# Kernel tuning notes

Hardware: AMD Instinct MI355X
Metric: run time of the kernel (lower is better)

## Reference

```python
import jax, jax.numpy as jnp
jax.config.update("jax_enable_x64", True)
import numpy as np

VOXEL_SIZE = 0.1   # size_scheduler.value
VBITS = 12         # bits per voxel coordinate (signed, offset by VOFF)
VMASK = (1 << VBITS) - 1
VOFF = 1 << (VBITS - 1)
GBITS = 10         # bits for group index (G=1024)


def setup_inputs() -> dict:
    key = jax.random.key(0)
    B, G, P, F = 64, 1024, 64, 3
    active_pred = jax.random.normal(key, (B * G, P, F), dtype=jnp.float32)
    active_mask = jnp.ones((B, G), dtype=bool)  # all active -> static nonzero count
    return {"active_pred": active_pred, "active_mask": active_mask}


def reference(active_pred, active_mask):
    N, P, F = active_pred.shape
    # active_mask.nonzero() -> [N, 2] (batch, group) ids
    bi, gi = jnp.nonzero(active_mask, size=N)
    bg = jnp.stack([bi, gi], axis=1).astype(jnp.int64)              # [N, 2]
    bg = jnp.broadcast_to(bg[:, None, :], (N, P, 2)).reshape(-1, 2)  # [N*P, 2]
    offsets = active_pred.reshape(-1, F)[:, :3]                      # [N*P, 3]
    vox = jnp.floor(offsets / VOXEL_SIZE).astype(jnp.int64)          # [N*P, 3]
    # Pack (b, g, vx, vy, vz) into one int64 key; packing is lexicographic-order
    # preserving, so sorted-unique of codes == torch.unique(dim=0) row order.
    v = vox + VOFF                                                   # nonnegative
    code = ((((bg[:, 0] << GBITS) | bg[:, 1]) << (3 * VBITS))
            | (v[:, 0] << (2 * VBITS)) | (v[:, 1] << VBITS) | v[:, 2])
    ucode, cluster_indices = jnp.unique(
        code, return_inverse=True, size=code.shape[0], fill_value=jnp.max(code))
    # Decode unique codes back to [U, 5] keys (padded tail repeats max key).
    ub = ucode >> (3 * VBITS + GBITS)
    ug = (ucode >> (3 * VBITS)) & ((1 << GBITS) - 1)
    uv0 = ((ucode >> (2 * VBITS)) & VMASK) - VOFF
    uv1 = ((ucode >> VBITS) & VMASK) - VOFF
    uv2 = (ucode & VMASK) - VOFF
    unique_keys = jnp.stack([ub, ug, uv0, uv1, uv2], axis=1)
    return unique_keys, cluster_indices
```

## Files before the change

### kernel.cpp

```cpp
#include <hip/hip_runtime.h>
#include <cstdint>

typedef unsigned long long u64;
typedef unsigned int u32;

constexpr int VBITS = 12;
constexpr int VOFF  = 1 << (VBITS - 1);
constexpr int GBITS = 10;

constexpr int GPB = 16;
constexpr int WPB = 4;
constexpr int GPW = 4;

__device__ inline u32 wave_sort_u32(u32 k, int lane) {
    #pragma unroll
    for (int ks = 2; ks <= 64; ks <<= 1) {
        #pragma unroll
        for (int j = ks >> 1; j >= 1; j >>= 1) {
            u32 other = __shfl_xor(k, j, 64);
            bool takeMin = ((lane & ks) == 0) == ((lane & j) == 0);
            u32 mn = min(k, other), mx = max(k, other);
            k = takeMin ? mn : mx;
        }
    }
    return k;
}

__device__ inline u64 wave_sort_u64(u64 k, int lane) {
    #pragma unroll
    for (int ks = 2; ks <= 64; ks <<= 1) {
        #pragma unroll
        for (int j = ks >> 1; j >= 1; j >>= 1) {
            u64 other = __shfl_xor(k, j, 64);
            bool takeMin = ((lane & ks) == 0) == ((lane & j) == 0);
            u64 mn = k < other ? k : other;
            u64 mx = k < other ? other : k;
            k = takeMin ? mn : mx;
        }
    }
    return k;
}

__device__ inline u64 voxel_code_u64(float x, float y, float z) {
    long long v0 = (long long)floorf(x / 0.1f) + VOFF;
    long long v1 = (long long)floorf(y / 0.1f) + VOFF;
    long long v2 = (long long)floorf(z / 0.1f) + VOFF;
    return ((u64)v0 << 24) | ((u64)v1 << 12) | (u64)v2;
}

__global__ __launch_bounds__(256) void vox_build(
    const float* __restrict__ pred,
    u32* __restrict__ keys32,
    u64* __restrict__ meta,
    u32* __restrict__ counts,
    u32* __restrict__ blockSums,
    int ngroups)
{
    __shared__ float sf[GPB * 192];
    __shared__ u32 s_ws[WPB];
    const int t = threadIdx.x, w = t >> 6, lane = t & 63, b = blockIdx.x;

    {
        const float4* p4 = (const float4*)pred + (size_t)b * (GPB * 48);
        const size_t f4tot = (size_t)ngroups * 48;
        float4* s4 = (float4*)sf;
        #pragma unroll
        for (int i = 0; i < 3; i++) {
            int idx = t + i * 256;
            size_t gidx = (size_t)b * (GPB * 48) + idx;
            if (gidx < f4tot) s4[idx] = p4[idx];
        }
    }
    __syncthreads();

    u32 wsum = 0;
    for (int j = 0; j < GPW; ++j) {
        int gi = w * GPW + j, gid = b * GPB + gi;
        if (gid >= ngroups) break;

        const float* q = sf + gi * 192 + lane * 3;
        int v0 = (int)floorf(q[0] / 0.1f) + VOFF;
        int v1 = (int)floorf(q[1] / 0.1f) + VOFF;
        int v2 = (int)floorf(q[2] / 0.1f) + VOFF;

        int r0 = __shfl(v0, 0, 64), r1 = __shfl(v1, 0, 64), r2 = __shfl(v2, 0, 64);
        int d0 = v0 - r0 + 128, d1 = v1 - r1 + 128, d2 = v2 - r2 + 128;
        bool bad = ((u32)(d0 | d1 | d2) > 255u) || ((u32)(v0 | v1 | v2) > 4095u);

        u32 cnt, outk;
        if (!__any(bad)) {
            u32 k = ((u32)d0 << 22) | ((u32)d1 << 14) | ((u32)d2 << 6) | (u32)lane;
            k = wave_sort_u32(k, lane);
            u32 sk = k >> 6, pv = __shfl_up(sk, 1, 64);
            int flag = (lane == 0 || sk != pv) ? 1 : 0;
            cnt = (u32)__popcll(__ballot(flag));
            outk = k;
            if (lane == 0)
                meta[gid] = ((u64)((u32)(r0 - 128) & 4095))
                          | ((u64)((u32)(r1 - 128) & 4095) << 12)
                          | ((u64)((u32)(r2 - 128) & 4095) << 24);
        } else {
            u64 code = ((u64)(long long)v0 << 24) | ((u64)(long long)v1 << 12)
                     | (u64)(long long)v2;
            u64 k = wave_sort_u64((code << 6) | (u64)lane, lane);
            u64 sk = k >> 6, pv = __shfl_up(sk, 1, 64);
            int flag = (lane == 0 || sk != pv) ? 1 : 0;
            cnt = (u32)__popcll(__ballot(flag));
            outk = (u32)(k & 63);
            if (lane == 0) meta[gid] = (1ull << 48);
        }
        keys32[(size_t)gid * 64 + lane] = outk;
        if (lane == 0) counts[gid] = cnt;
        wsum += cnt;
    }
    if (lane == 0) s_ws[w] = wsum;
    __syncthreads();
    if (t == 0) blockSums[b] = s_ws[0] + s_ws[1] + s_ws[2] + s_ws[3];
}

__global__ __launch_bounds__(256) void vox_emit(
    const float* __restrict__ pred,
    const u32* __restrict__ keys32,
    const u64* __restrict__ meta,
    const u32* __restrict__ counts,
    const u32* __restrict__ blockSums,
    int* __restrict__ okeys,
    int* __restrict__ inv,
    int ngroups, int totalrows, int nblocks)
{
    __shared__ u32 s_k[GPB * 64];
    __shared__ u32 s_c[GPB];
    __shared__ u64 s_m[GPB];
    __shared__ int s_stage[WPB][320];
    __shared__ u32 s_baseU[2];
    __shared__ int s_tail[5];
    const int t = threadIdx.x, w = t >> 6, lane = t & 63, b = blockIdx.x;

    {
        const uint4* k4 = (const uint4*)keys32 + (size_t)b * (GPB * 16);
        const size_t k4tot = (size_t)ngroups * 16;
        size_t gidx = (size_t)b * (GPB * 16) + t;
        if (gidx < k4tot) ((uint4*)s_k)[t] = k4[t];
    }
    if (t < GPB) {
        int gid = b * GPB + t;
        s_c[t] = (gid < ngroups) ? counts[gid] : 0;
        s_m[t] = (gid < ngroups) ? meta[gid] : 0;
    }

    {
        u32 below = 0, all = 0;
        for (int i = t; i < nblocks; i += 256) {
            u32 v = blockSums[i];
            all += v;
            if (i < b) below += v;
        }
        u32* scratch = (u32*)&s_stage[0][0];
        scratch[t] = below; scratch[256 + t] = all;
        __syncthreads();
        #pragma unroll
        for (int off = 128; off >= 1; off >>= 1) {
            if (t < off) {
                scratch[t]       += scratch[t + off];
                scratch[256 + t] += scratch[256 + t + off];
            }
            __syncthreads();
        }
        if (t == 0) { s_baseU[0] = scratch[0]; s_baseU[1] = scratch[256]; }
        __syncthreads();
    }

    u32 base = s_baseU[0];
    #pragma unroll
    for (int i = 0; i < GPB; i++) if (i < w * GPW) base += s_c[i];

    for (int j = 0; j < GPW; ++j) {
        int gi = w * GPW + j, gid = b * GPB + gi;
        if (gid >= ngroups) break;

        u32 kk = s_k[gi * 64 + lane];
        u64 m  = s_m[gi];
        int orig = (int)(kk & 63);
        int flag, vd0, vd1, vd2;

        if (!((m >> 48) & 1)) {
            u32 sk = kk >> 6, pv = __shfl_up(sk, 1, 64);
            flag = (lane == 0 || sk != pv) ? 1 : 0;
            u32 d0 = (kk >> 22) & 255, d1 = (kk >> 14) & 255, d2 = (kk >> 6) & 255;
            u32 m0 = (u32)m & 4095, m1 = (u32)(m >> 12) & 4095, m2 = (u32)(m >> 24) & 4095;
            vd0 = (int)((m0 + d0) & 4095);
            vd1 = (int)((m1 + d1) & 4095);
            vd2 = (int)((m2 + d2) & 4095);
        } else {
            const float* p = pred + (size_t)gid * 192 + orig * 3;
            u64 scode = voxel_code_u64(p[0], p[1], p[2]);
            u64 pv = __shfl_up(scode, 1, 64);
            flag = (lane == 0 || scode != pv) ? 1 : 0;
            vd0 = (int)((scode >> 24) & 4095);
            vd1 = (int)((scode >> 12) & 4095);
            vd2 = (int)(scode & 4095);
        }

        u64 bal = __ballot(flag);
        int rank = (int)__popcll(bal & ((1ull << lane) - 1ull)) + flag - 1;
        u32 cnt = s_c[gi];

        inv[(size_t)gid * 64 + orig] = (int)(base + (u32)rank);

        int* buf = s_stage[w];
        if (flag) {
            buf[rank * 5 + 0] = gid >> GBITS;
            buf[rank * 5 + 1] = gid & ((1 << GBITS) - 1);
            buf[rank * 5 + 2] = vd0 - VOFF;
            buf[rank * 5 + 3] = vd1 - VOFF;
            buf[rank * 5 + 4] = vd2 - VOFF;
        }
        u32 n5 = cnt * 5;
        int* dst = okeys + (size_t)base * 5;
        for (u32 i = lane; i < n5; i += 64) dst[i] = buf[i];
        base += cnt;
    }

    if (w == 0) {
        int lg = ngroups - 1;
        const float* p = pred + (size_t)lg * 192 + lane * 3;
        u64 code = voxel_code_u64(p[0], p[1], p[2]);
        #pragma unroll
        for (int off = 32; off >= 1; off >>= 1) {
            u64 o = __shfl_xor(code, off, 64);
            code = (o > code) ? o : code;
        }
        if (lane == 0) {
            s_tail[0] = lg >> GBITS;
            s_tail[1] = lg & ((1 << GBITS) - 1);
            s_tail[2] = (int)((code >> 24) & 4095) - VOFF;
            s_tail[3] = (int)((code >> 12) & 4095) - VOFF;
            s_tail[4] = (int)(code & 4095) - VOFF;
        }
    }
    __syncthreads();
    {
        u32 U = s_baseU[1];
        u32 total5 = (u32)totalrows * 5u;
        u32 stride = (u32)gridDim.x * 256u;
        for (u32 e = U * 5u + (u32)b * 256u + (u32)t; e < total5; e += stride)
            okeys[e] = s_tail[e % 5u];
    }
}

extern "C" void kernel_launch(void* const* d_in, const int* in_sizes, int n_in,
                              void* d_out, int out_size, void* d_ws, size_t ws_size,
                              hipStream_t stream)
{
    const float* pred = (const float*)d_in[0];
    int ngroups   = in_sizes[1];
    int totalrows = in_sizes[0] / 3;
    int nblocks   = (ngroups + GPB - 1) / GPB;

    int* okeys = (int*)d_out;
    int* inv   = okeys + (size_t)totalrows * 5;

    char* ws = (char*)d_ws;
    u64* meta      = (u64*)ws;
    u32* keys32    = (u32*)(meta + ngroups);
    u32* counts    = keys32 + (size_t)ngroups * 64;
    u32* blockSums = counts + ngroups;

    vox_build<<<nblocks, 256, 0, stream>>>(pred, keys32, meta, counts,
                                           blockSums, ngroups);
    vox_emit<<<nblocks, 256, 0, stream>>>(pred, keys32, meta, counts, blockSums,
                                          okeys, inv, ngroups, totalrows, nblocks);
}
```

Baseline: 56.82 us.

## Count uniques with shared hash table and recompute sort in emit pass

The first kernel now only counts unique voxels per group, using a per-group LDS open-addressing hash table with atomicCAS in place of the bitonic sort, and no longer writes sorted keys or metadata to the workspace. The emit kernel reloads the raw predictions and redoes the voxelization and wave sort itself. This removes the intermediate keys32/meta global round trip in exchange for doing the sort twice in total work terms and adding LDS atomics in the count pass.

```diff
diff --git a/kernel.cpp b/kernel.cpp
--- a/kernel.cpp
+++ b/kernel.cpp
@@ -41,25 +41,19 @@
     return k;
 }
 
-__device__ inline u64 voxel_code_u64(float x, float y, float z) {
-    long long v0 = (long long)floorf(x / 0.1f) + VOFF;
-    long long v1 = (long long)floorf(y / 0.1f) + VOFF;
-    long long v2 = (long long)floorf(z / 0.1f) + VOFF;
-    return ((u64)v0 << 24) | ((u64)v1 << 12) | (u64)v2;
-}
-
-__global__ __launch_bounds__(256) void vox_build(
+__global__ __launch_bounds__(256) void vox_count(
     const float* __restrict__ pred,
-    u32* __restrict__ keys32,
-    u64* __restrict__ meta,
     u32* __restrict__ counts,
     u32* __restrict__ blockSums,
     int ngroups)
 {
     __shared__ float sf[GPB * 192];
+    __shared__ u32 tab[GPB][128];
     __shared__ u32 s_ws[WPB];
     const int t = threadIdx.x, w = t >> 6, lane = t & 63, b = blockIdx.x;
 
+    #pragma unroll
+    for (int i = 0; i < (GPB * 128) / 256; i++) tab[0][t + i * 256] = 0;
     {
         const float4* p4 = (const float4*)pred + (size_t)b * (GPB * 48);
         const size_t f4tot = (size_t)ngroups * 48;
@@ -67,8 +61,7 @@
         #pragma unroll
         for (int i = 0; i < 3; i++) {
             int idx = t + i * 256;
-            size_t gidx = (size_t)b * (GPB * 48) + idx;
-            if (gidx < f4tot) s4[idx] = p4[idx];
+            if ((size_t)b * (GPB * 48) + idx < f4tot) s4[idx] = p4[idx];
         }
     }
     __syncthreads();
@@ -76,42 +69,38 @@
     u32 wsum = 0;
     for (int j = 0; j < GPW; ++j) {
         int gi = w * GPW + j, gid = b * GPB + gi;
-        if (gid >= ngroups) break;
-
-        const float* q = sf + gi * 192 + lane * 3;
-        int v0 = (int)floorf(q[0] / 0.1f) + VOFF;
-        int v1 = (int)floorf(q[1] / 0.1f) + VOFF;
-        int v2 = (int)floorf(q[2] / 0.1f) + VOFF;
-
-        int r0 = __shfl(v0, 0, 64), r1 = __shfl(v1, 0, 64), r2 = __shfl(v2, 0, 64);
-        int d0 = v0 - r0 + 128, d1 = v1 - r1 + 128, d2 = v2 - r2 + 128;
-        bool bad = ((u32)(d0 | d1 | d2) > 255u) || ((u32)(v0 | v1 | v2) > 4095u);
-
-        u32 cnt, outk;
-        if (!__any(bad)) {
-            u32 k = ((u32)d0 << 22) | ((u32)d1 << 14) | ((u32)d2 << 6) | (u32)lane;
-            k = wave_sort_u32(k, lane);
-            u32 sk = k >> 6, pv = __shfl_up(sk, 1, 64);
-            int flag = (lane == 0 || sk != pv) ? 1 : 0;
-            cnt = (u32)__popcll(__ballot(flag));
-            outk = k;
-            if (lane == 0)
-                meta[gid] = ((u64)((u32)(r0 - 128) & 4095))
-                          | ((u64)((u32)(r1 - 128) & 4095) << 12)
-                          | ((u64)((u32)(r2 - 128) & 4095) << 24);
-        } else {
-            u64 code = ((u64)(long long)v0 << 24) | ((u64)(long long)v1 << 12)
-                     | (u64)(long long)v2;
-            u64 k = wave_sort_u64((code << 6) | (u64)lane, lane);
-            u64 sk = k >> 6, pv = __shfl_up(sk, 1, 64);
-            int flag = (lane == 0 || sk != pv) ? 1 : 0;
-            cnt = (u32)__popcll(__ballot(flag));
-            outk = (u32)(k & 63);
-            if (lane == 0) meta[gid] = (1ull << 48);
-        }
-        keys32[(size_t)gid * 64 + lane] = outk;
-        if (lane == 0) counts[gid] = cnt;
-        wsum += cnt;
+        if (gid < ngroups) {
+            const float* q = sf + gi * 192 + lane * 3;
+            int v0 = (int)floorf(q[0] / 0.1f) + VOFF;
+            int v1 = (int)floorf(q[1] / 0.1f) + VOFF;
+            int v2 = (int)floorf(q[2] / 0.1f) + VOFF;
+            int r0 = __shfl(v0, 0, 64), r1 = __shfl(v1, 0, 64), r2 = __shfl(v2, 0, 64);
+            int d0 = v0 - r0 + 128, d1 = v1 - r1 + 128, d2 = v2 - r2 + 128;
+            bool bad = ((u32)(d0 | d1 | d2) > 255u) || ((u32)(v0 | v1 | v2) > 4095u);
+
+            u32 cnt;
+            if (!__any(bad)) {
+                u32 key = (((u32)d0 << 16) | ((u32)d1 << 8) | (u32)d2) | 0x80000000u;
+                u32 slot = ((key * 2654435761u) >> 25) & 127u;
+                bool inserted = false;
+                while (true) {
+                    u32 old = atomicCAS(&tab[gi][slot], 0u, key);
+                    if (old == 0u) { inserted = true; break; }
+                    if (old == key) break;
+                    slot = (slot + 1) & 127u;
+                }
+                cnt = (u32)__popcll(__ballot(inserted));
+            } else {
+                u64 code = ((u64)(long long)v0 << 24) | ((u64)(long long)v1 << 12)
+                         | (u64)(long long)v2;
+                u64 k = wave_sort_u64((code << 6) | (u64)lane, lane);
+                u64 sk = k >> 6, pv = __shfl_up(sk, 1, 64);
+                int flag = (lane == 0 || sk != pv) ? 1 : 0;
+                cnt = (u32)__popcll(__ballot(flag));
+            }
+            if (lane == 0) counts[gid] = cnt;
+            wsum += cnt;
+        }
     }
     if (lane == 0) s_ws[w] = wsum;
     __syncthreads();
@@ -120,32 +109,32 @@
 
 __global__ __launch_bounds__(256) void vox_emit(
     const float* __restrict__ pred,
-    const u32* __restrict__ keys32,
-    const u64* __restrict__ meta,
     const u32* __restrict__ counts,
     const u32* __restrict__ blockSums,
     int* __restrict__ okeys,
     int* __restrict__ inv,
     int ngroups, int totalrows, int nblocks)
 {
-    __shared__ u32 s_k[GPB * 64];
+    __shared__ float sf[GPB * 192];
+    __shared__ int s_stage[WPB][320];
     __shared__ u32 s_c[GPB];
-    __shared__ u64 s_m[GPB];
-    __shared__ int s_stage[WPB][320];
     __shared__ u32 s_baseU[2];
     __shared__ int s_tail[5];
     const int t = threadIdx.x, w = t >> 6, lane = t & 63, b = blockIdx.x;
 
     {
-        const uint4* k4 = (const uint4*)keys32 + (size_t)b * (GPB * 16);
-        const size_t k4tot = (size_t)ngroups * 16;
-        size_t gidx = (size_t)b * (GPB * 16) + t;
-        if (gidx < k4tot) ((uint4*)s_k)[t] = k4[t];
+        const float4* p4 = (const float4*)pred + (size_t)b * (GPB * 48);
+        const size_t f4tot = (size_t)ngroups * 48;
+        float4* s4 = (float4*)sf;
+        #pragma unroll
+        for (int i = 0; i < 3; i++) {
+            int idx = t + i * 256;
+            if ((size_t)b * (GPB * 48) + idx < f4tot) s4[idx] = p4[idx];
+        }
     }
     if (t < GPB) {
         int gid = b * GPB + t;
         s_c[t] = (gid < ngroups) ? counts[gid] : 0;
-        s_m[t] = (gid < ngroups) ? meta[gid] : 0;
     }
 
     {
@@ -156,6 +145,7 @@
             if (i < b) below += v;
         }
         u32* scratch = (u32*)&s_stage[0][0];
+        __syncthreads();
         scratch[t] = below; scratch[256 + t] = all;
         __syncthreads();
         #pragma unroll
@@ -176,55 +166,65 @@
 
     for (int j = 0; j < GPW; ++j) {
         int gi = w * GPW + j, gid = b * GPB + gi;
-        if (gid >= ngroups) break;
-
-        u32 kk = s_k[gi * 64 + lane];
-        u64 m  = s_m[gi];
-        int orig = (int)(kk & 63);
-        int flag, vd0, vd1, vd2;
-
-        if (!((m >> 48) & 1)) {
-            u32 sk = kk >> 6, pv = __shfl_up(sk, 1, 64);
-            flag = (lane == 0 || sk != pv) ? 1 : 0;
-            u32 d0 = (kk >> 22) & 255, d1 = (kk >> 14) & 255, d2 = (kk >> 6) & 255;
-            u32 m0 = (u32)m & 4095, m1 = (u32)(m >> 12) & 4095, m2 = (u32)(m >> 24) & 4095;
-            vd0 = (int)((m0 + d0) & 4095);
-            vd1 = (int)((m1 + d1) & 4095);
-            vd2 = (int)((m2 + d2) & 4095);
-        } else {
-            const float* p = pred + (size_t)gid * 192 + orig * 3;
-            u64 scode = voxel_code_u64(p[0], p[1], p[2]);
-            u64 pv = __shfl_up(scode, 1, 64);
-            flag = (lane == 0 || scode != pv) ? 1 : 0;
-            vd0 = (int)((scode >> 24) & 4095);
-            vd1 = (int)((scode >> 12) & 4095);
-            vd2 = (int)(scode & 4095);
-        }
-
-        u64 bal = __ballot(flag);
-        int rank = (int)__popcll(bal & ((1ull << lane) - 1ull)) + flag - 1;
-        u32 cnt = s_c[gi];
-
-        inv[(size_t)gid * 64 + orig] = (int)(base + (u32)rank);
-
-        int* buf = s_stage[w];
-        if (flag) {
-            buf[rank * 5 + 0] = gid >> GBITS;
-            buf[rank * 5 + 1] = gid & ((1 << GBITS) - 1);
-            buf[rank * 5 + 2] = vd0 - VOFF;
-            buf[rank * 5 + 3] = vd1 - VOFF;
-            buf[rank * 5 + 4] = vd2 - VOFF;
-        }
-        u32 n5 = cnt * 5;
-        int* dst = okeys + (size_t)base * 5;
-        for (u32 i = lane; i < n5; i += 64) dst[i] = buf[i];
-        base += cnt;
+        if (gid < ngroups) {
+            const float* q = sf + gi * 192 + lane * 3;
+            int v0 = (int)floorf(q[0] / 0.1f) + VOFF;
+            int v1 = (int)floorf(q[1] / 0.1f) + VOFF;
+            int v2 = (int)floorf(q[2] / 0.1f) + VOFF;
+            int r0 = __shfl(v0, 0, 64), r1 = __shfl(v1, 0, 64), r2 = __shfl(v2, 0, 64);
+            int d0 = v0 - r0 + 128, d1 = v1 - r1 + 128, d2 = v2 - r2 + 128;
+            bool bad = ((u32)(d0 | d1 | d2) > 255u) || ((u32)(v0 | v1 | v2) > 4095u);
+
+            int orig, flag, vd0, vd1, vd2;
+            if (!__any(bad)) {
+                u32 k = ((u32)d0 << 22) | ((u32)d1 << 14) | ((u32)d2 << 6) | (u32)lane;
+                k = wave_sort_u32(k, lane);
+                u32 sk = k >> 6, pv = __shfl_up(sk, 1, 64);
+                flag = (lane == 0 || sk != pv) ? 1 : 0;
+                orig = (int)(k & 63);
+                vd0 = (r0 - 128) + (int)((k >> 22) & 255);
+                vd1 = (r1 - 128) + (int)((k >> 14) & 255);
+                vd2 = (r2 - 128) + (int)((k >> 6) & 255);
+            } else {
+                u64 code = ((u64)(long long)v0 << 24) | ((u64)(long long)v1 << 12)
+                         | (u64)(long long)v2;
+                u64 k = wave_sort_u64((code << 6) | (u64)lane, lane);
+                u64 sk = k >> 6, pv = __shfl_up(sk, 1, 64);
+                flag = (lane == 0 || sk != pv) ? 1 : 0;
+                orig = (int)(k & 63);
+                vd0 = (int)((sk >> 24) & 4095);
+                vd1 = (int)((sk >> 12) & 4095);
+                vd2 = (int)(sk & 4095);
+            }
+
+            u64 bal = __ballot(flag);
+            int rank = (int)__popcll(bal & ((1ull << lane) - 1ull)) + flag - 1;
+            u32 cnt = (u32)__popcll(bal);
+
+            inv[(size_t)gid * 64 + orig] = (int)(base + (u32)rank);
+
+            int* buf = s_stage[w];
+            if (flag) {
+                buf[rank * 5 + 0] = gid >> GBITS;
+                buf[rank * 5 + 1] = gid & ((1 << GBITS) - 1);
+                buf[rank * 5 + 2] = vd0 - VOFF;
+                buf[rank * 5 + 3] = vd1 - VOFF;
+                buf[rank * 5 + 4] = vd2 - VOFF;
+            }
+            u32 n5 = cnt * 5;
+            int* dst = okeys + (size_t)base * 5;
+            for (u32 i = lane; i < n5; i += 64) dst[i] = buf[i];
+            base += cnt;
+        }
     }
 
     if (w == 0) {
         int lg = ngroups - 1;
         const float* p = pred + (size_t)lg * 192 + lane * 3;
-        u64 code = voxel_code_u64(p[0], p[1], p[2]);
+        long long w0 = (long long)floorf(p[0] / 0.1f) + VOFF;
+        long long w1 = (long long)floorf(p[1] / 0.1f) + VOFF;
+        long long w2 = (long long)floorf(p[2] / 0.1f) + VOFF;
+        u64 code = ((u64)w0 << 24) | ((u64)w1 << 12) | (u64)w2;
         #pragma unroll
         for (int off = 32; off >= 1; off >>= 1) {
             u64 o = __shfl_xor(code, off, 64);
@@ -260,14 +260,10 @@
     int* okeys = (int*)d_out;
     int* inv   = okeys + (size_t)totalrows * 5;
 
-    char* ws = (char*)d_ws;
-    u64* meta      = (u64*)ws;
-    u32* keys32    = (u32*)(meta + ngroups);
-    u32* counts    = keys32 + (size_t)ngroups * 64;
+    u32* counts    = (u32*)d_ws;
     u32* blockSums = counts + ngroups;
 
-    vox_build<<<nblocks, 256, 0, stream>>>(pred, keys32, meta, counts,
-                                           blockSums, ngroups);
-    vox_emit<<<nblocks, 256, 0, stream>>>(pred, keys32, meta, counts, blockSums,
+    vox_count<<<nblocks, 256, 0, stream>>>(pred, counts, blockSums, ngroups);
+    vox_emit<<<nblocks, 256, 0, stream>>>(pred, counts, blockSums,
                                           okeys, inv, ngroups, totalrows, nblocks);
 }
```

After: 69.83 us. 1.23x slower.

## Precompute ranks and compacted unique keys in build, fold counts into meta

Applied to the files above, without the earlier changes.

The build kernel now computes each point's rank and a compacted list of unique delta keys, using shared-memory scatter. It packs them into one u32 per lane, and the count goes into the meta word. The emit kernel then writes inverse indices coalesced by lane and no longer recomputes flags, ballots or the shared key tile. This drops the separate counts array and moves the scatter work out of the second pass, which should shorten emit. The cost is more shared-memory traffic in build, plus an added sync before the scratch reuse.

```diff
diff --git a/kernel.cpp b/kernel.cpp
--- a/kernel.cpp
+++ b/kernel.cpp
@@ -41,22 +41,16 @@
     return k;
 }
 
-__device__ inline u64 voxel_code_u64(float x, float y, float z) {
-    long long v0 = (long long)floorf(x / 0.1f) + VOFF;
-    long long v1 = (long long)floorf(y / 0.1f) + VOFF;
-    long long v2 = (long long)floorf(z / 0.1f) + VOFF;
-    return ((u64)v0 << 24) | ((u64)v1 << 12) | (u64)v2;
-}
-
 __global__ __launch_bounds__(256) void vox_build(
     const float* __restrict__ pred,
-    u32* __restrict__ keys32,
+    u32* __restrict__ arr,
     u64* __restrict__ meta,
-    u32* __restrict__ counts,
     u32* __restrict__ blockSums,
     int ngroups)
 {
     __shared__ float sf[GPB * 192];
+    __shared__ u32 s_d[WPB][64];
+    __shared__ u32 s_r[WPB][64];
     __shared__ u32 s_ws[WPB];
     const int t = threadIdx.x, w = t >> 6, lane = t & 63, b = blockIdx.x;
 
@@ -67,8 +61,7 @@
         #pragma unroll
         for (int i = 0; i < 3; i++) {
             int idx = t + i * 256;
-            size_t gidx = (size_t)b * (GPB * 48) + idx;
-            if (gidx < f4tot) s4[idx] = p4[idx];
+            if ((size_t)b * (GPB * 48) + idx < f4tot) s4[idx] = p4[idx];
         }
     }
     __syncthreads();
@@ -76,42 +69,54 @@
     u32 wsum = 0;
     for (int j = 0; j < GPW; ++j) {
         int gi = w * GPW + j, gid = b * GPB + gi;
-        if (gid >= ngroups) break;
-
-        const float* q = sf + gi * 192 + lane * 3;
-        int v0 = (int)floorf(q[0] / 0.1f) + VOFF;
-        int v1 = (int)floorf(q[1] / 0.1f) + VOFF;
-        int v2 = (int)floorf(q[2] / 0.1f) + VOFF;
-
-        int r0 = __shfl(v0, 0, 64), r1 = __shfl(v1, 0, 64), r2 = __shfl(v2, 0, 64);
-        int d0 = v0 - r0 + 128, d1 = v1 - r1 + 128, d2 = v2 - r2 + 128;
-        bool bad = ((u32)(d0 | d1 | d2) > 255u) || ((u32)(v0 | v1 | v2) > 4095u);
-
-        u32 cnt, outk;
-        if (!__any(bad)) {
-            u32 k = ((u32)d0 << 22) | ((u32)d1 << 14) | ((u32)d2 << 6) | (u32)lane;
-            k = wave_sort_u32(k, lane);
-            u32 sk = k >> 6, pv = __shfl_up(sk, 1, 64);
-            int flag = (lane == 0 || sk != pv) ? 1 : 0;
-            cnt = (u32)__popcll(__ballot(flag));
-            outk = k;
-            if (lane == 0)
-                meta[gid] = ((u64)((u32)(r0 - 128) & 4095))
-                          | ((u64)((u32)(r1 - 128) & 4095) << 12)
-                          | ((u64)((u32)(r2 - 128) & 4095) << 24);
-        } else {
-            u64 code = ((u64)(long long)v0 << 24) | ((u64)(long long)v1 << 12)
-                     | (u64)(long long)v2;
-            u64 k = wave_sort_u64((code << 6) | (u64)lane, lane);
-            u64 sk = k >> 6, pv = __shfl_up(sk, 1, 64);
-            int flag = (lane == 0 || sk != pv) ? 1 : 0;
-            cnt = (u32)__popcll(__ballot(flag));
-            outk = (u32)(k & 63);
-            if (lane == 0) meta[gid] = (1ull << 48);
-        }
-        keys32[(size_t)gid * 64 + lane] = outk;
-        if (lane == 0) counts[gid] = cnt;
-        wsum += cnt;
+        if (gid < ngroups) {
+            const float* q = sf + gi * 192 + lane * 3;
+            int v0 = (int)floorf(q[0] / 0.1f) + VOFF;
+            int v1 = (int)floorf(q[1] / 0.1f) + VOFF;
+            int v2 = (int)floorf(q[2] / 0.1f) + VOFF;
+            int r0 = __shfl(v0, 0, 64), r1 = __shfl(v1, 0, 64), r2 = __shfl(v2, 0, 64);
+            int d0 = v0 - r0 + 128, d1 = v1 - r1 + 128, d2 = v2 - r2 + 128;
+            bool bad = ((u32)(d0 | d1 | d2) > 255u) || ((u32)(v0 | v1 | v2) > 4095u);
+
+            u32 cnt, packed;
+            if (!__any(bad)) {
+                u32 k = ((u32)d0 << 22) | ((u32)d1 << 14) | ((u32)d2 << 6) | (u32)lane;
+                k = wave_sort_u32(k, lane);
+                u32 sk = k >> 6;
+                u32 pv = __shfl_up(sk, 1, 64);
+                int flag = (lane == 0 || sk != pv) ? 1 : 0;
+                u64 bal = __ballot(flag);
+                int rank = (int)__popcll(bal & ((1ull << lane) - 1ull)) + flag - 1;
+                cnt = (u32)__popcll(bal);
+                int orig = (int)(k & 63);
+
+                s_d[w][lane] = 0;
+                if (flag) s_d[w][rank] = sk;
+                s_r[w][orig] = (u32)rank;
+                packed = s_d[w][lane] | (s_r[w][lane] << 24);
+
+                if (lane == 0)
+                    meta[gid] = ((u64)((u32)(r0 - 128) & 4095))
+                              | ((u64)((u32)(r1 - 128) & 4095) << 12)
+                              | ((u64)((u32)(r2 - 128) & 4095) << 24)
+                              | ((u64)cnt << 48);
+            } else {
+                u64 code = ((u64)(long long)v0 << 24) | ((u64)(long long)v1 << 12)
+                         | (u64)(long long)v2;
+                u64 k = wave_sort_u64((code << 6) | (u64)lane, lane);
+                u64 sk = k >> 6, pv = __shfl_up(sk, 1, 64);
+                int flag = (lane == 0 || sk != pv) ? 1 : 0;
+                u64 bal = __ballot(flag);
+                int rank = (int)__popcll(bal & ((1ull << lane) - 1ull)) + flag - 1;
+                cnt = (u32)__popcll(bal);
+                int orig = (int)(k & 63);
+                s_r[w][orig] = (u32)rank;
+                packed = s_r[w][lane] << 24;
+                if (lane == 0) meta[gid] = ((u64)cnt << 48) | (1ull << 56);
+            }
+            arr[(size_t)gid * 64 + lane] = packed;
+            wsum += cnt;
+        }
     }
     if (lane == 0) s_ws[w] = wsum;
     __syncthreads();
@@ -120,32 +125,23 @@
 
 __global__ __launch_bounds__(256) void vox_emit(
     const float* __restrict__ pred,
-    const u32* __restrict__ keys32,
+    const u32* __restrict__ arr,
     const u64* __restrict__ meta,
-    const u32* __restrict__ counts,
     const u32* __restrict__ blockSums,
     int* __restrict__ okeys,
     int* __restrict__ inv,
     int ngroups, int totalrows, int nblocks)
 {
-    __shared__ u32 s_k[GPB * 64];
+    __shared__ int s_stage[WPB][320];
+    __shared__ u64 s_code[WPB][64];
     __shared__ u32 s_c[GPB];
-    __shared__ u64 s_m[GPB];
-    __shared__ int s_stage[WPB][320];
     __shared__ u32 s_baseU[2];
     __shared__ int s_tail[5];
     const int t = threadIdx.x, w = t >> 6, lane = t & 63, b = blockIdx.x;
 
-    {
-        const uint4* k4 = (const uint4*)keys32 + (size_t)b * (GPB * 16);
-        const size_t k4tot = (size_t)ngroups * 16;
-        size_t gidx = (size_t)b * (GPB * 16) + t;
-        if (gidx < k4tot) ((uint4*)s_k)[t] = k4[t];
-    }
     if (t < GPB) {
         int gid = b * GPB + t;
-        s_c[t] = (gid < ngroups) ? counts[gid] : 0;
-        s_m[t] = (gid < ngroups) ? meta[gid] : 0;
+        s_c[t] = (gid < ngroups) ? (u32)((meta[gid] >> 48) & 127) : 0;
     }
 
     {
@@ -156,6 +152,7 @@
             if (i < b) below += v;
         }
         u32* scratch = (u32*)&s_stage[0][0];
+        __syncthreads();
         scratch[t] = below; scratch[256 + t] = all;
         __syncthreads();
         #pragma unroll
@@ -176,55 +173,56 @@
 
     for (int j = 0; j < GPW; ++j) {
         int gi = w * GPW + j, gid = b * GPB + gi;
-        if (gid >= ngroups) break;
-
-        u32 kk = s_k[gi * 64 + lane];
-        u64 m  = s_m[gi];
-        int orig = (int)(kk & 63);
-        int flag, vd0, vd1, vd2;
-
-        if (!((m >> 48) & 1)) {
-            u32 sk = kk >> 6, pv = __shfl_up(sk, 1, 64);
-            flag = (lane == 0 || sk != pv) ? 1 : 0;
-            u32 d0 = (kk >> 22) & 255, d1 = (kk >> 14) & 255, d2 = (kk >> 6) & 255;
-            u32 m0 = (u32)m & 4095, m1 = (u32)(m >> 12) & 4095, m2 = (u32)(m >> 24) & 4095;
-            vd0 = (int)((m0 + d0) & 4095);
-            vd1 = (int)((m1 + d1) & 4095);
-            vd2 = (int)((m2 + d2) & 4095);
-        } else {
-            const float* p = pred + (size_t)gid * 192 + orig * 3;
-            u64 scode = voxel_code_u64(p[0], p[1], p[2]);
-            u64 pv = __shfl_up(scode, 1, 64);
-            flag = (lane == 0 || scode != pv) ? 1 : 0;
-            vd0 = (int)((scode >> 24) & 4095);
-            vd1 = (int)((scode >> 12) & 4095);
-            vd2 = (int)(scode & 4095);
-        }
-
-        u64 bal = __ballot(flag);
-        int rank = (int)__popcll(bal & ((1ull << lane) - 1ull)) + flag - 1;
-        u32 cnt = s_c[gi];
-
-        inv[(size_t)gid * 64 + orig] = (int)(base + (u32)rank);
-
-        int* buf = s_stage[w];
-        if (flag) {
-            buf[rank * 5 + 0] = gid >> GBITS;
-            buf[rank * 5 + 1] = gid & ((1 << GBITS) - 1);
-            buf[rank * 5 + 2] = vd0 - VOFF;
-            buf[rank * 5 + 3] = vd1 - VOFF;
-            buf[rank * 5 + 4] = vd2 - VOFF;
-        }
-        u32 n5 = cnt * 5;
-        int* dst = okeys + (size_t)base * 5;
-        for (u32 i = lane; i < n5; i += 64) dst[i] = buf[i];
-        base += cnt;
+        if (gid < ngroups) {
+            u64 m = meta[gid];
+            u32 a = arr[(size_t)gid * 64 + lane];
+            u32 cnt = (u32)((m >> 48) & 127);
+            u32 rinv = a >> 24;
+
+            inv[(size_t)gid * 64 + lane] = (int)(base + rinv);
+
+            int vd0 = 0, vd1 = 0, vd2 = 0;
+            if (!((m >> 56) & 1)) {
+                u32 d = a & 0xFFFFFFu;
+                u32 m0 = (u32)m & 4095, m1 = (u32)(m >> 12) & 4095, m2 = (u32)(m >> 24) & 4095;
+                vd0 = (int)((m0 + ((d >> 16) & 255)) & 4095);
+                vd1 = (int)((m1 + ((d >> 8) & 255)) & 4095);
+                vd2 = (int)((m2 + (d & 255)) & 4095);
+            } else {
+                const float* p = pred + (size_t)gid * 192 + lane * 3;
+                long long w0 = (long long)floorf(p[0] / 0.1f) + VOFF;
+                long long w1 = (long long)floorf(p[1] / 0.1f) + VOFF;
+                long long w2 = (long long)floorf(p[2] / 0.1f) + VOFF;
+                u64 code = ((u64)w0 << 24) | ((u64)w1 << 12) | (u64)w2;
+                s_code[w][rinv] = code;
+                u64 c = s_code[w][lane];
+                vd0 = (int)((c >> 24) & 4095);
+                vd1 = (int)((c >> 12) & 4095);
+                vd2 = (int)(c & 4095);
+            }
+
+            int* buf = s_stage[w];
+            if (lane < (int)cnt) {
+                buf[lane * 5 + 0] = gid >> GBITS;
+                buf[lane * 5 + 1] = gid & ((1 << GBITS) - 1);
+                buf[lane * 5 + 2] = vd0 - VOFF;
+                buf[lane * 5 + 3] = vd1 - VOFF;
+                buf[lane * 5 + 4] = vd2 - VOFF;
+            }
+            u32 n5 = cnt * 5;
+            int* dst = okeys + (size_t)base * 5;
+            for (u32 i = lane; i < n5; i += 64) dst[i] = buf[i];
+            base += cnt;
+        }
     }
 
     if (w == 0) {
         int lg = ngroups - 1;
         const float* p = pred + (size_t)lg * 192 + lane * 3;
-        u64 code = voxel_code_u64(p[0], p[1], p[2]);
+        long long w0 = (long long)floorf(p[0] / 0.1f) + VOFF;
+        long long w1 = (long long)floorf(p[1] / 0.1f) + VOFF;
+        long long w2 = (long long)floorf(p[2] / 0.1f) + VOFF;
+        u64 code = ((u64)w0 << 24) | ((u64)w1 << 12) | (u64)w2;
         #pragma unroll
         for (int off = 32; off >= 1; off >>= 1) {
             u64 o = __shfl_xor(code, off, 64);
@@ -262,12 +260,10 @@
 
     char* ws = (char*)d_ws;
     u64* meta      = (u64*)ws;
-    u32* keys32    = (u32*)(meta + ngroups);
-    u32* counts    = keys32 + (size_t)ngroups * 64;
-    u32* blockSums = counts + ngroups;
-
-    vox_build<<<nblocks, 256, 0, stream>>>(pred, keys32, meta, counts,
-                                           blockSums, ngroups);
-    vox_emit<<<nblocks, 256, 0, stream>>>(pred, keys32, meta, counts, blockSums,
+    u32* arr       = (u32*)(meta + ngroups);
+    u32* blockSums = arr + (size_t)ngroups * 64;
+
+    vox_build<<<nblocks, 256, 0, stream>>>(pred, arr, meta, blockSums, ngroups);
+    vox_emit<<<nblocks, 256, 0, stream>>>(pred, arr, meta, blockSums,
                                           okeys, inv, ngroups, totalrows, nblocks);
 }
```

After: 59.10 us. +4.0%, slower.
